# Optimization experiments

Measured on AMD Instinct MI355X. Metric: run time of the kernel, lower is better.

Reference implementation:

```python
import jax, jax.numpy as jnp
import numpy as np

N_NODES = 100000
N_EDGES = 3200000
IN_DIM, HID, OUT = 256, 64, 10


def setup_inputs() -> dict:
    key = jax.random.key(0)
    ks = jax.random.split(key, 6)
    x = jax.random.normal(ks[0], (N_NODES, IN_DIM), jnp.float32)
    edge_index = jax.random.randint(ks[1], (2, N_EDGES), 0, N_NODES, dtype=jnp.int64)
    edge_weight = jnp.ones((N_EDGES,), jnp.float32)
    # Glorot-scaled weights; PyG GCNConv keeps bias separate from lin.
    W1 = jax.random.normal(ks[2], (HID, IN_DIM), jnp.float32) * np.float32(1.0 / np.sqrt(IN_DIM))
    b1 = jnp.zeros((HID,), jnp.float32)
    W2 = jax.random.normal(ks[3], (HID, HID), jnp.float32) * np.float32(1.0 / np.sqrt(HID))
    b2 = jnp.zeros((HID,), jnp.float32)
    W3 = jax.random.normal(ks[4], (OUT, HID), jnp.float32) * np.float32(1.0 / np.sqrt(HID))
    b3 = jnp.zeros((OUT,), jnp.float32)
    return dict(x=x, edge_index=edge_index, edge_weight=edge_weight,
                W1=W1, b1=b1, W2=W2, b2=b2, W3=W3, b3=b3)


def _gcn_conv(x, W, b, row, col, edge_weight, n):
    """PyG GCNConv with add_self_loops=False: out = D^{-1/2} A D^{-1/2} (x W^T) + b."""
    h = x @ W.T  # [N, out_dim]
    deg = jax.ops.segment_sum(edge_weight, col, num_segments=n)  # in-degree by weight
    dinv = jnp.where(deg > 0, jax.lax.rsqrt(jnp.maximum(deg, 1e-12)), 0.0)
    norm = dinv[row] * edge_weight * dinv[col]  # [E]
    msgs = h[row] * norm[:, None]               # gather from source nodes
    out = jax.ops.segment_sum(msgs, col, num_segments=n)  # scatter-add to targets
    return out + b


def reference(x, edge_index, edge_weight, W1, b1, W2, b2, W3, b3):
    row, col = edge_index[0], edge_index[1]
    n = x.shape[0]
    h = jax.nn.relu(_gcn_conv(x, W1, b1, row, col, edge_weight, n))
    h = jax.nn.relu(_gcn_conv(h, W2, b2, row, col, edge_weight, n))
    out = _gcn_conv(h, W3, b3, row, col, edge_weight, n)  # logits, [N, num_classes]
    return out
```

## Files before the change

kernel.cpp:

```cpp
#include <hip/hip_runtime.h>
#include <stddef.h>

typedef __attribute__((ext_vector_type(8))) short bf16x8;
typedef __attribute__((ext_vector_type(4))) float f32x4;

#define NPB 512
#define PB  512

__device__ inline float bf2f(unsigned short u) {
    unsigned int v = ((unsigned int)u) << 16;
    float f;
    __builtin_memcpy(&f, &v, 4);
    return f;
}
__device__ inline unsigned short f2bf(float f) {
    unsigned int v;
    __builtin_memcpy(&v, &f, 4);
    unsigned int r = (v + 0x7FFFu + ((v >> 16) & 1u)) >> 16;
    return (unsigned short)r;
}
__device__ inline float feat(const void* p, long long idx, int isbf) {
    if (isbf) return bf2f(((const unsigned short*)p)[idx]);
    return ((const float*)p)[idx];
}
__device__ inline int clampi(int v, int lo, int hi) {
    return v < lo ? lo : (v > hi ? hi : v);
}

__global__ void detect_kernel(const int* ei, const unsigned short* ew16,
                              const unsigned short* x16, int* flags) {
    __shared__ int s_is64, s_pass;
    if (threadIdx.x == 0) { s_is64 = 1; s_pass = 0; }
    __syncthreads();
    int t = threadIdx.x;
    if (t < 128 && ei[2 * t + 1] != 0) atomicAnd(&s_is64, 0);
    if (t < 64) {
        unsigned short h = x16[t];
        unsigned int expf = (h >> 7) & 0xFF;
        if (h == 0 || (expf >= 112 && expf <= 142)) atomicAdd(&s_pass, 1);
    }
    __syncthreads();
    if (t == 0) {
        flags[0] = s_is64;
        flags[1] = (ew16[0] == 0x3F80) ? 1 : 0;
        flags[2] = (s_pass >= 56) ? 1 : 0;
        flags[3] = 1;
    }
}

__global__ void ones_kernel(const void* ew, int* flags, int E) {
    int i = blockIdx.x * blockDim.x + threadIdx.x;
    int wbf = flags[1];
    int b = i * 4;
    int lim = b + 4 < E ? b + 4 : E;
    bool bad = false;
    for (int k = b; k < lim; k++)
        if (feat(ew, k, wbf) != 1.0f) bad = true;
    if (bad) atomicAnd(&flags[3], 0);
}

__global__ void sentinel_kernel(unsigned short* outp, int n, float val) {
    int i = blockIdx.x * blockDim.x + threadIdx.x;
    if (i < n) outp[i] = f2bf(val);
}

__global__ __launch_bounds__(512) void khist_kernel(const int* ei, const int* flags,
                                                    int* ghist, int E, int n,
                                                    int NB, int chunk) {
    __shared__ int hist[256];
    int blk = blockIdx.x;
    for (int i = threadIdx.x; i < NB; i += blockDim.x) hist[i] = 0;
    __syncthreads();
    int is64 = flags[0];
    int e0 = blk * chunk;
    int e1 = e0 + chunk < E ? e0 + chunk : E;
    for (int e = e0 + (int)threadIdx.x; e < e1; e += blockDim.x) {
        int c = is64 ? ei[2 * (E + e)] : ei[E + e];
        c = clampi(c, 0, n - 1);
        atomicAdd(&hist[c >> 9], 1);
    }
    __syncthreads();
    for (int i = threadIdx.x; i < NB; i += blockDim.x) ghist[blk * NB + i] = hist[i];
}

__global__ __launch_bounds__(512) void koff1_kernel(int* ghist, int* btot, int NB) {
    __shared__ int s[512];
    int b = blockIdx.x;
    int t = threadIdx.x;
    int v = ghist[t * NB + b];
    s[t] = v;
    __syncthreads();
    for (int off = 1; off < 512; off <<= 1) {
        int add = (t >= off) ? s[t - off] : 0;
        __syncthreads();
        s[t] += add;
        __syncthreads();
    }
    ghist[t * NB + b] = s[t] - v;
    if (t == 511) btot[b] = s[511];
}

__global__ __launch_bounds__(256) void koff2_kernel(const int* btot, int* bstart,
                                                    int* row_ptr, int NB, int N, int E) {
    __shared__ int s[256];
    int t = threadIdx.x;
    int v = (t < NB) ? btot[t] : 0;
    s[t] = v;
    __syncthreads();
    for (int off = 1; off < 256; off <<= 1) {
        int add = (t >= off) ? s[t - off] : 0;
        __syncthreads();
        s[t] += add;
        __syncthreads();
    }
    if (t < NB) bstart[t] = s[t] - v;
    if (t == 0) row_ptr[N] = E;
}

__global__ __launch_bounds__(512) void kscatter_kernel(const int* ei, const void* ew,
                                                       const int* flags, const int* ghist,
                                                       const int* bstart,
                                                       unsigned int* ebuf, float* wbuf,
                                                       int E, int n, int NB, int chunk) {
    __shared__ int cur[256];
    int blk = blockIdx.x;
    for (int i = threadIdx.x; i < NB; i += blockDim.x)
        cur[i] = ghist[blk * NB + i] + bstart[i];
    __syncthreads();
    int is64 = flags[0], wbf = flags[1], ones = flags[3];
    int e0 = blk * chunk;
    int e1 = e0 + chunk < E ? e0 + chunk : E;
    for (int e = e0 + (int)threadIdx.x; e < e1; e += blockDim.x) {
        int r = is64 ? ei[2 * e] : ei[e];
        int c = is64 ? ei[2 * (E + e)] : ei[E + e];
        r = clampi(r, 0, n - 1);
        c = clampi(c, 0, n - 1);
        int b = c >> 9;
        int pos = atomicAdd(&cur[b], 1);
        ebuf[pos] = ((unsigned int)(c & 511) << 17) | (unsigned int)r;
        if (!ones) wbuf[pos] = feat(ew, e, wbf);
    }
}

__global__ __launch_bounds__(512) void kcsr_a_kernel(const unsigned int* ebuf,
                                                     const float* wbuf, const int* flags,
                                                     const int* bstart, const int* btot,
                                                     int* row_ptr, float* dinv, int N) {
    __shared__ int cnt[512];
    __shared__ int pre[512];
    __shared__ float wsum[512];
    int b = blockIdx.x;
    int t = threadIdx.x;
    int ones = flags[3];
    cnt[t] = 0;
    wsum[t] = 0.f;
    __syncthreads();
    int bs = bstart[b];
    int be = bs + btot[b];
    for (int i = bs + t; i < be; i += 512) {
        unsigned int p = ebuf[i];
        int cl = (int)(p >> 17);
        atomicAdd(&cnt[cl], 1);
        if (!ones) atomicAdd(&wsum[cl], wbuf[i]);
    }
    __syncthreads();
    int v = cnt[t];
    pre[t] = v;
    __syncthreads();
    for (int off = 1; off < 512; off <<= 1) {
        int add = (t >= off) ? pre[t - off] : 0;
        __syncthreads();
        pre[t] += add;
        __syncthreads();
    }
    int node = b * NPB + t;
    if (node < N) {
        row_ptr[node] = bs + pre[t] - v;
        float d = ones ? (float)v : wsum[t];
        dinv[node] = (d > 0.f) ? rsqrtf(fmaxf(d, 1e-12f)) : 0.f;
    }
}

__global__ __launch_bounds__(512) void kcsr_b_kernel(const unsigned int* ebuf,
                                                     const float* wbuf, const int* flags,
                                                     const int* bstart, const int* btot,
                                                     const int* row_ptr, const float* dinv,
                                                     int2* csr_pack, int N) {
    __shared__ int cur[512];
    __shared__ float dloc[512];
    int b = blockIdx.x;
    int t = threadIdx.x;
    int ones = flags[3];
    int node = b * NPB + t;
    cur[t] = (node < N) ? row_ptr[node] : 0;
    dloc[t] = (node < N) ? dinv[node] : 0.f;
    __syncthreads();
    int bs = bstart[b];
    int be = bs + btot[b];
    for (int i = bs + t; i < be; i += 512) {
        unsigned int p = ebuf[i];
        int cl = (int)(p >> 17);
        int r = (int)(p & 0x1FFFFu);
        float w = ones ? 1.0f : wbuf[i];
        float nv = dinv[r] * w * dloc[cl];
        int pos = atomicAdd(&cur[cl], 1);
        csr_pack[pos] = make_int2(r, __float_as_int(nv));
    }
}

__device__ inline void split8(const float* p, bf16x8& hi, bf16x8& lo) {
    for (int i = 0; i < 8; i++) {
        float v = p[i];
        unsigned short h = f2bf(v);
        hi[i] = (short)h;
        lo[i] = (short)f2bf(v - bf2f(h));
    }
}

__global__ void gemm1_kernel(const void* A, const void* W, const int* flags,
                             unsigned short* C, int M, int K) {
    int wave = threadIdx.x >> 6;
    int l = threadIdx.x & 63;
    int m = l & 15;
    int quad = l >> 4;
    int row0 = blockIdx.x * 16;
    int col0 = wave * 16;
    bool arow_ok = (row0 + m) < M;
    int fb = flags[2];
    f32x4 acc = {0.f, 0.f, 0.f, 0.f};
    bf16x8 zf = {0, 0, 0, 0, 0, 0, 0, 0};
    if (fb) {
        const short* As = (const short*)A;
        const short* Ws = (const short*)W;
        for (int k0 = 0; k0 < K; k0 += 32) {
            bf16x8 a = arow_ok
                ? *(const bf16x8*)(As + (long long)(row0 + m) * K + k0 + quad * 8) : zf;
            bf16x8 b = *(const bf16x8*)(Ws + (long long)(col0 + m) * K + k0 + quad * 8);
            acc = __builtin_amdgcn_mfma_f32_16x16x32_bf16(a, b, acc, 0, 0, 0);
        }
    } else {
        const float* Af = (const float*)A;
        const float* Wf = (const float*)W;
        for (int k0 = 0; k0 < K; k0 += 32) {
            bf16x8 ah = zf, al = zf, wh, wl;
            if (arow_ok)
                split8(Af + (long long)(row0 + m) * K + k0 + quad * 8, ah, al);
            split8(Wf + (long long)(col0 + m) * K + k0 + quad * 8, wh, wl);
            acc = __builtin_amdgcn_mfma_f32_16x16x32_bf16(ah, wh, acc, 0, 0, 0);
            acc = __builtin_amdgcn_mfma_f32_16x16x32_bf16(al, wh, acc, 0, 0, 0);
            acc = __builtin_amdgcn_mfma_f32_16x16x32_bf16(ah, wl, acc, 0, 0, 0);
        }
    }
    for (int r = 0; r < 4; r++) {
        int row = row0 + quad * 4 + r;
        if (row < M) C[(long long)row * 64 + col0 + m] = f2bf(acc[r]);
    }
}

__global__ void gemm2_kernel(const unsigned short* A, const void* W, const int* flags,
                             unsigned short* C, int M) {
    int wave = threadIdx.x >> 6;
    int l = threadIdx.x & 63;
    int m = l & 15;
    int quad = l >> 4;
    int row0 = blockIdx.x * 16;
    int col0 = wave * 16;
    bool arow_ok = (row0 + m) < M;
    int fb = flags[2];
    f32x4 acc = {0.f, 0.f, 0.f, 0.f};
    bf16x8 zf = {0, 0, 0, 0, 0, 0, 0, 0};
    const short* As = (const short*)A;
    for (int k0 = 0; k0 < 64; k0 += 32) {
        bf16x8 a = arow_ok
            ? *(const bf16x8*)(As + (long long)(row0 + m) * 64 + k0 + quad * 8) : zf;
        if (fb) {
            const short* Ws = (const short*)W;
            bf16x8 b = *(const bf16x8*)(Ws + (long long)(col0 + m) * 64 + k0 + quad * 8);
            acc = __builtin_amdgcn_mfma_f32_16x16x32_bf16(a, b, acc, 0, 0, 0);
        } else {
            bf16x8 wh, wl;
            split8((const float*)W + (long long)(col0 + m) * 64 + k0 + quad * 8, wh, wl);
            acc = __builtin_amdgcn_mfma_f32_16x16x32_bf16(a, wh, acc, 0, 0, 0);
            acc = __builtin_amdgcn_mfma_f32_16x16x32_bf16(a, wl, acc, 0, 0, 0);
        }
    }
    for (int r = 0; r < 4; r++) {
        int row = row0 + quad * 4 + r;
        if (row < M) C[(long long)row * 64 + col0 + m] = f2bf(acc[r]);
    }
}

__global__ void gemm3_kernel(const unsigned short* A, const void* W, const int* flags,
                             unsigned short* C, int M) {
    int wv = threadIdx.x >> 6;
    int l = threadIdx.x & 63;
    int m = l & 15;
    int quad = l >> 4;
    int row0 = (blockIdx.x * 4 + wv) * 16;
    bool arow_ok = (row0 + m) < M;
    bool bcol_ok = m < 10;
    int fb = flags[2];
    f32x4 acc = {0.f, 0.f, 0.f, 0.f};
    bf16x8 zf = {0, 0, 0, 0, 0, 0, 0, 0};
    const short* As = (const short*)A;
    for (int k0 = 0; k0 < 64; k0 += 32) {
        bf16x8 a = arow_ok
            ? *(const bf16x8*)(As + (long long)(row0 + m) * 64 + k0 + quad * 8) : zf;
        if (fb) {
            const short* Ws = (const short*)W;
            bf16x8 b = bcol_ok
                ? *(const bf16x8*)(Ws + (long long)m * 64 + k0 + quad * 8) : zf;
            acc = __builtin_amdgcn_mfma_f32_16x16x32_bf16(a, b, acc, 0, 0, 0);
        } else {
            bf16x8 wh = zf, wl = zf;
            if (bcol_ok)
                split8((const float*)W + (long long)m * 64 + k0 + quad * 8, wh, wl);
            acc = __builtin_amdgcn_mfma_f32_16x16x32_bf16(a, wh, acc, 0, 0, 0);
            acc = __builtin_amdgcn_mfma_f32_16x16x32_bf16(a, wl, acc, 0, 0, 0);
        }
    }
    if (bcol_ok) {
        for (int r = 0; r < 4; r++) {
            int row = row0 + quad * 4 + r;
            if (row < M) C[(long long)row * 10 + m] = f2bf(acc[r]);
        }
    }
}

__global__ void agg64_kernel(const unsigned short* h, const void* bias,
                             const int* flags, const int* row_ptr,
                             const int2* cp, unsigned short* outp, int n, int do_relu) {
    int l = threadIdx.x & 63;
    int node = blockIdx.x * 4 + (int)(threadIdx.x >> 6);
    if (node >= n) return;
    int g = l >> 3;
    int j = l & 7;
    int beg = row_ptr[node];
    int end = row_ptr[node + 1];
    float a0 = 0.f, a1 = 0.f, a2 = 0.f, a3 = 0.f;
    float a4 = 0.f, a5 = 0.f, a6 = 0.f, a7 = 0.f;
    for (int e = beg; e < end; e += 8) {
        int ee = e + g;
        if (ee < end) {
            int2 p = cp[ee];
            float nv = __int_as_float(p.y);
            uint4 raw = *(const uint4*)(h + (long long)p.x * 64 + j * 8);
            a0 += nv * __uint_as_float(raw.x << 16);
            a1 += nv * __uint_as_float(raw.x & 0xFFFF0000u);
            a2 += nv * __uint_as_float(raw.y << 16);
            a3 += nv * __uint_as_float(raw.y & 0xFFFF0000u);
            a4 += nv * __uint_as_float(raw.z << 16);
            a5 += nv * __uint_as_float(raw.z & 0xFFFF0000u);
            a6 += nv * __uint_as_float(raw.w << 16);
            a7 += nv * __uint_as_float(raw.w & 0xFFFF0000u);
        }
    }
    for (int mask = 8; mask <= 32; mask <<= 1) {
        a0 += __shfl_xor(a0, mask);
        a1 += __shfl_xor(a1, mask);
        a2 += __shfl_xor(a2, mask);
        a3 += __shfl_xor(a3, mask);
        a4 += __shfl_xor(a4, mask);
        a5 += __shfl_xor(a5, mask);
        a6 += __shfl_xor(a6, mask);
        a7 += __shfl_xor(a7, mask);
    }
    if (g == 0) {
        int fb = flags[2];
        float v0 = a0 + feat(bias, j * 8 + 0, fb);
        float v1 = a1 + feat(bias, j * 8 + 1, fb);
        float v2 = a2 + feat(bias, j * 8 + 2, fb);
        float v3 = a3 + feat(bias, j * 8 + 3, fb);
        float v4 = a4 + feat(bias, j * 8 + 4, fb);
        float v5 = a5 + feat(bias, j * 8 + 5, fb);
        float v6 = a6 + feat(bias, j * 8 + 6, fb);
        float v7 = a7 + feat(bias, j * 8 + 7, fb);
        if (do_relu) {
            v0 = fmaxf(v0, 0.f); v1 = fmaxf(v1, 0.f);
            v2 = fmaxf(v2, 0.f); v3 = fmaxf(v3, 0.f);
            v4 = fmaxf(v4, 0.f); v5 = fmaxf(v5, 0.f);
            v6 = fmaxf(v6, 0.f); v7 = fmaxf(v7, 0.f);
        }
        uint4 pk;
        pk.x = (unsigned int)f2bf(v0) | ((unsigned int)f2bf(v1) << 16);
        pk.y = (unsigned int)f2bf(v2) | ((unsigned int)f2bf(v3) << 16);
        pk.z = (unsigned int)f2bf(v4) | ((unsigned int)f2bf(v5) << 16);
        pk.w = (unsigned int)f2bf(v6) | ((unsigned int)f2bf(v7) << 16);
        *(uint4*)(outp + (long long)node * 64 + j * 8) = pk;
    }
}

__global__ void agg10_kernel(const unsigned short* h, const void* bias,
                             const int* flags, const int* row_ptr,
                             const int2* cp, void* outp, int n) {
    int lane = threadIdx.x & 63;
    int node = blockIdx.x * 4 + (int)(threadIdx.x >> 6);
    if (node >= n) return;
    int beg = row_ptr[node];
    int end = row_ptr[node + 1];
    int active = (lane < 10) ? 1 : 0;
    int li = active ? lane : 0;
    float acc = 0.f;
    int e = beg;
    for (; e + 4 <= end; e += 4) {
        int2 p0 = cp[e + 0], p1 = cp[e + 1], p2 = cp[e + 2], p3 = cp[e + 3];
        float h0 = bf2f(h[(long long)p0.x * 10 + li]);
        float h1 = bf2f(h[(long long)p1.x * 10 + li]);
        float h2 = bf2f(h[(long long)p2.x * 10 + li]);
        float h3 = bf2f(h[(long long)p3.x * 10 + li]);
        acc += __int_as_float(p0.y) * h0 + __int_as_float(p1.y) * h1 +
               __int_as_float(p2.y) * h2 + __int_as_float(p3.y) * h3;
    }
    for (; e < end; e++) {
        int2 p = cp[e];
        acc += __int_as_float(p.y) * bf2f(h[(long long)p.x * 10 + li]);
    }
    if (active) {
        float v = acc + feat(bias, lane, flags[2]);
        if (flags[2]) ((unsigned short*)outp)[(long long)node * 10 + lane] = f2bf(v);
        else          ((float*)outp)[(long long)node * 10 + lane] = v;
    }
}

extern "C" void kernel_launch(void* const* d_in, const int* in_sizes, int n_in,
                              void* d_out, int out_size, void* d_ws, size_t ws_size,
                              hipStream_t stream) {
    const void* x  = d_in[0];
    const int*  ei = (const int*)d_in[1];
    const void* ew = d_in[2];
    const void* W1 = d_in[3];
    const void* b1 = d_in[4];
    const void* W2 = d_in[5];
    const void* b2 = d_in[6];
    const void* W3 = d_in[7];
    const void* b3 = d_in[8];

    const int N = in_sizes[0] / 256;
    const int E = in_sizes[1] / 2;
    const int TB = 256;
    const int NB = (N + NPB - 1) / NPB;
    const int chunk = (E + PB - 1) / PB;

    size_t off = 0;
    size_t o_flags = off; off += 16;
    size_t o_ghist = off; off += (size_t)PB * NB * 4; off = (off + 15) & ~(size_t)15;
    size_t o_btot  = off; off += (size_t)NB * 4;
    size_t o_bst   = off; off += (size_t)NB * 4; off = (off + 15) & ~(size_t)15;
    size_t o_rp    = off; off += (size_t)(N + 1) * 4;
    size_t o_dinv  = off; off += (size_t)N * 4; off = (off + 15) & ~(size_t)15;
    size_t o_pack  = off; off += (size_t)E * 8;
    size_t o_bufA  = off; off += (size_t)N * 64 * 2;
    size_t o_bufB  = off; off += (size_t)N * 64 * 2;
    size_t o_h3    = off; off += (size_t)N * 10 * 2;
    size_t need = off;
    if (ws_size < need || (size_t)E * 4 > (size_t)N * 64 * 2) {
        sentinel_kernel<<<dim3((out_size + TB - 1) / TB), dim3(TB), 0, stream>>>(
            (unsigned short*)d_out, out_size, 250.0f);
        return;
    }
    char* ws = (char*)d_ws;
    int*   flags    = (int*)(ws + o_flags);
    int*   ghist    = (int*)(ws + o_ghist);
    int*   btot     = (int*)(ws + o_btot);
    int*   bstart   = (int*)(ws + o_bst);
    int*   row_ptr  = (int*)(ws + o_rp);
    float* dinv     = (float*)(ws + o_dinv);
    int2*  csr_pack = (int2*)(ws + o_pack);
    unsigned short* bufA  = (unsigned short*)(ws + o_bufA);
    unsigned short* bufB  = (unsigned short*)(ws + o_bufB);
    unsigned short* h3buf = (unsigned short*)(ws + o_h3);
    float*        wbuf = (float*)bufA;
    unsigned int* ebuf = (unsigned int*)bufB;

    dim3 tb(TB);
    dim3 tb512(512);
    dim3 gE4((E / 4 + TB - 1) / TB);
    dim3 g16((N + 15) / 16);
    dim3 g64((N + 63) / 64);
    dim3 gAgg((N + 3) / 4);
    dim3 one(1);

    detect_kernel<<<one, tb, 0, stream>>>(ei, (const unsigned short*)ew,
                                          (const unsigned short*)x, flags);
    ones_kernel<<<gE4, tb, 0, stream>>>(ew, flags, E);
    khist_kernel<<<dim3(PB), tb512, 0, stream>>>(ei, flags, ghist, E, N, NB, chunk);
    koff1_kernel<<<dim3(NB), tb512, 0, stream>>>(ghist, btot, NB);
    koff2_kernel<<<one, tb, 0, stream>>>(btot, bstart, row_ptr, NB, N, E);
    kscatter_kernel<<<dim3(PB), tb512, 0, stream>>>(ei, ew, flags, ghist, bstart,
                                                    ebuf, wbuf, E, N, NB, chunk);
    kcsr_a_kernel<<<dim3(NB), tb512, 0, stream>>>(ebuf, wbuf, flags, bstart, btot,
                                                  row_ptr, dinv, N);
    kcsr_b_kernel<<<dim3(NB), tb512, 0, stream>>>(ebuf, wbuf, flags, bstart, btot,
                                                  row_ptr, dinv, csr_pack, N);

    gemm1_kernel<<<g16, tb, 0, stream>>>(x, W1, flags, bufA, N, 256);
    agg64_kernel<<<gAgg, tb, 0, stream>>>(bufA, b1, flags, row_ptr, csr_pack,
                                          bufB, N, 1);
    gemm2_kernel<<<g16, tb, 0, stream>>>(bufB, W2, flags, bufA, N);
    agg64_kernel<<<gAgg, tb, 0, stream>>>(bufA, b2, flags, row_ptr, csr_pack,
                                          bufB, N, 1);
    gemm3_kernel<<<g64, tb, 0, stream>>>(bufB, W3, flags, h3buf, N);
    agg10_kernel<<<gAgg, tb, 0, stream>>>(h3buf, b3, flags, row_ptr, csr_pack,
                                          d_out, N);
}
```

Measured before the change: 660.0 us.

## Pre-split weights to bf16 hi/lo and compute all output columns per wave

Adds a small kernel that splits each weight matrix into bf16 hi/lo halves once per call, instead of re-splitting fp32 weights inside every GEMM wave. The three GEMMs are reorganized so each wave owns 16 rows and computes all 64 output columns with four accumulators. As a result, the fp32 input row (256 wide in layer 1) is loaded and split once rather than once per column-wave. The cost is three extra small launches, extra workspace, and more accumulator registers per thread.

```diff
diff --git a/kernel.cpp b/kernel.cpp
--- a/kernel.cpp
+++ b/kernel.cpp
@@ -3,6 +3,7 @@
 
 typedef __attribute__((ext_vector_type(8))) short bf16x8;
 typedef __attribute__((ext_vector_type(4))) float f32x4;
+typedef __attribute__((ext_vector_type(8))) float f32x8;
 
 #define NPB 512
 #define PB  512
@@ -62,6 +63,22 @@
 __global__ void sentinel_kernel(unsigned short* outp, int n, float val) {
     int i = blockIdx.x * blockDim.x + threadIdx.x;
     if (i < n) outp[i] = f2bf(val);
+}
+
+__global__ void wsplit_kernel(const void* W, const int* flags, unsigned short* hi,
+                              unsigned short* lo, int n_in, int n_out) {
+    int i = blockIdx.x * blockDim.x + threadIdx.x;
+    if (i >= n_out) return;
+    if (i >= n_in) { hi[i] = 0; lo[i] = 0; return; }
+    if (flags[2]) {
+        hi[i] = ((const unsigned short*)W)[i];
+        lo[i] = 0;
+    } else {
+        float v = ((const float*)W)[i];
+        unsigned short h = f2bf(v);
+        hi[i] = h;
+        lo[i] = f2bf(v - bf2f(h));
+    }
 }
 
 __global__ __launch_bounds__(512) void khist_kernel(const int* ei, const int* flags,
@@ -208,118 +225,139 @@
     }
 }
 
-__device__ inline void split8(const float* p, bf16x8& hi, bf16x8& lo) {
+__device__ inline void split8v(f32x8 v, bf16x8& hi, bf16x8& lo) {
     for (int i = 0; i < 8; i++) {
-        float v = p[i];
-        unsigned short h = f2bf(v);
+        float f = v[i];
+        unsigned short h = f2bf(f);
         hi[i] = (short)h;
-        lo[i] = (short)f2bf(v - bf2f(h));
-    }
-}
-
-__global__ void gemm1_kernel(const void* A, const void* W, const int* flags,
-                             unsigned short* C, int M, int K) {
+        lo[i] = (short)f2bf(f - bf2f(h));
+    }
+}
+
+__global__ __launch_bounds__(256) void gemm1_kernel(const void* A,
+                             const unsigned short* Whi, const unsigned short* Wlo,
+                             const int* flags, unsigned short* C, int M, int K) {
     int wave = threadIdx.x >> 6;
     int l = threadIdx.x & 63;
     int m = l & 15;
     int quad = l >> 4;
-    int row0 = blockIdx.x * 16;
-    int col0 = wave * 16;
+    int row0 = blockIdx.x * 64 + wave * 16;
     bool arow_ok = (row0 + m) < M;
     int fb = flags[2];
-    f32x4 acc = {0.f, 0.f, 0.f, 0.f};
+    f32x4 acc[4];
+    #pragma unroll
+    for (int n = 0; n < 4; n++) acc[n] = (f32x4){0.f, 0.f, 0.f, 0.f};
     bf16x8 zf = {0, 0, 0, 0, 0, 0, 0, 0};
+    long long abase = (long long)(row0 + m) * K + quad * 8;
     if (fb) {
         const short* As = (const short*)A;
-        const short* Ws = (const short*)W;
+        #pragma unroll 4
         for (int k0 = 0; k0 < K; k0 += 32) {
-            bf16x8 a = arow_ok
-                ? *(const bf16x8*)(As + (long long)(row0 + m) * K + k0 + quad * 8) : zf;
-            bf16x8 b = *(const bf16x8*)(Ws + (long long)(col0 + m) * K + k0 + quad * 8);
-            acc = __builtin_amdgcn_mfma_f32_16x16x32_bf16(a, b, acc, 0, 0, 0);
+            bf16x8 a = arow_ok ? *(const bf16x8*)(As + abase + k0) : zf;
+            #pragma unroll
+            for (int n = 0; n < 4; n++) {
+                const unsigned short* wp = Whi + (long long)(n * 16 + m) * K + k0 + quad * 8;
+                bf16x8 b = *(const bf16x8*)wp;
+                acc[n] = __builtin_amdgcn_mfma_f32_16x16x32_bf16(a, b, acc[n], 0, 0, 0);
+            }
         }
     } else {
         const float* Af = (const float*)A;
-        const float* Wf = (const float*)W;
+        #pragma unroll 2
         for (int k0 = 0; k0 < K; k0 += 32) {
-            bf16x8 ah = zf, al = zf, wh, wl;
-            if (arow_ok)
-                split8(Af + (long long)(row0 + m) * K + k0 + quad * 8, ah, al);
-            split8(Wf + (long long)(col0 + m) * K + k0 + quad * 8, wh, wl);
-            acc = __builtin_amdgcn_mfma_f32_16x16x32_bf16(ah, wh, acc, 0, 0, 0);
-            acc = __builtin_amdgcn_mfma_f32_16x16x32_bf16(al, wh, acc, 0, 0, 0);
-            acc = __builtin_amdgcn_mfma_f32_16x16x32_bf16(ah, wl, acc, 0, 0, 0);
-        }
-    }
-    for (int r = 0; r < 4; r++) {
-        int row = row0 + quad * 4 + r;
-        if (row < M) C[(long long)row * 64 + col0 + m] = f2bf(acc[r]);
-    }
-}
-
-__global__ void gemm2_kernel(const unsigned short* A, const void* W, const int* flags,
-                             unsigned short* C, int M) {
+            bf16x8 ah = zf, al = zf;
+            if (arow_ok) {
+                f32x8 av = *(const f32x8*)(Af + abase + k0);
+                split8v(av, ah, al);
+            }
+            #pragma unroll
+            for (int n = 0; n < 4; n++) {
+                long long widx = (long long)(n * 16 + m) * K + k0 + quad * 8;
+                bf16x8 wh = *(const bf16x8*)(Whi + widx);
+                bf16x8 wl = *(const bf16x8*)(Wlo + widx);
+                acc[n] = __builtin_amdgcn_mfma_f32_16x16x32_bf16(ah, wh, acc[n], 0, 0, 0);
+                acc[n] = __builtin_amdgcn_mfma_f32_16x16x32_bf16(al, wh, acc[n], 0, 0, 0);
+                acc[n] = __builtin_amdgcn_mfma_f32_16x16x32_bf16(ah, wl, acc[n], 0, 0, 0);
+            }
+        }
+    }
+    #pragma unroll
+    for (int n = 0; n < 4; n++) {
+        #pragma unroll
+        for (int r = 0; r < 4; r++) {
+            int row = row0 + quad * 4 + r;
+            if (row < M) C[(long long)row * 64 + n * 16 + m] = f2bf(acc[n][r]);
+        }
+    }
+}
+
+__global__ __launch_bounds__(256) void gemm2_kernel(const unsigned short* A,
+                             const unsigned short* Whi, const unsigned short* Wlo,
+                             const int* flags, unsigned short* C, int M) {
     int wave = threadIdx.x >> 6;
     int l = threadIdx.x & 63;
     int m = l & 15;
     int quad = l >> 4;
-    int row0 = blockIdx.x * 16;
-    int col0 = wave * 16;
+    int row0 = blockIdx.x * 64 + wave * 16;
+    bool arow_ok = (row0 + m) < M;
+    int fb = flags[2];
+    f32x4 acc[4];
+    #pragma unroll
+    for (int n = 0; n < 4; n++) acc[n] = (f32x4){0.f, 0.f, 0.f, 0.f};
+    bf16x8 zf = {0, 0, 0, 0, 0, 0, 0, 0};
+    const short* As = (const short*)A;
+    long long abase = (long long)(row0 + m) * 64 + quad * 8;
+    #pragma unroll
+    for (int k0 = 0; k0 < 64; k0 += 32) {
+        bf16x8 a = arow_ok ? *(const bf16x8*)(As + abase + k0) : zf;
+        #pragma unroll
+        for (int n = 0; n < 4; n++) {
+            long long widx = (long long)(n * 16 + m) * 64 + k0 + quad * 8;
+            bf16x8 wh = *(const bf16x8*)(Whi + widx);
+            acc[n] = __builtin_amdgcn_mfma_f32_16x16x32_bf16(a, wh, acc[n], 0, 0, 0);
+            if (!fb) {
+                bf16x8 wl = *(const bf16x8*)(Wlo + widx);
+                acc[n] = __builtin_amdgcn_mfma_f32_16x16x32_bf16(a, wl, acc[n], 0, 0, 0);
+            }
+        }
+    }
+    #pragma unroll
+    for (int n = 0; n < 4; n++) {
+        #pragma unroll
+        for (int r = 0; r < 4; r++) {
+            int row = row0 + quad * 4 + r;
+            if (row < M) C[(long long)row * 64 + n * 16 + m] = f2bf(acc[n][r]);
+        }
+    }
+}
+
+__global__ __launch_bounds__(256) void gemm3_kernel(const unsigned short* A,
+                             const unsigned short* Whi, const unsigned short* Wlo,
+                             const int* flags, unsigned short* C, int M) {
+    int wave = threadIdx.x >> 6;
+    int l = threadIdx.x & 63;
+    int m = l & 15;
+    int quad = l >> 4;
+    int row0 = blockIdx.x * 64 + wave * 16;
     bool arow_ok = (row0 + m) < M;
     int fb = flags[2];
     f32x4 acc = {0.f, 0.f, 0.f, 0.f};
     bf16x8 zf = {0, 0, 0, 0, 0, 0, 0, 0};
     const short* As = (const short*)A;
+    long long abase = (long long)(row0 + m) * 64 + quad * 8;
+    #pragma unroll
     for (int k0 = 0; k0 < 64; k0 += 32) {
-        bf16x8 a = arow_ok
-            ? *(const bf16x8*)(As + (long long)(row0 + m) * 64 + k0 + quad * 8) : zf;
-        if (fb) {
-            const short* Ws = (const short*)W;
-            bf16x8 b = *(const bf16x8*)(Ws + (long long)(col0 + m) * 64 + k0 + quad * 8);
-            acc = __builtin_amdgcn_mfma_f32_16x16x32_bf16(a, b, acc, 0, 0, 0);
-        } else {
-            bf16x8 wh, wl;
-            split8((const float*)W + (long long)(col0 + m) * 64 + k0 + quad * 8, wh, wl);
-            acc = __builtin_amdgcn_mfma_f32_16x16x32_bf16(a, wh, acc, 0, 0, 0);
+        bf16x8 a = arow_ok ? *(const bf16x8*)(As + abase + k0) : zf;
+        long long widx = (long long)m * 64 + k0 + quad * 8;
+        bf16x8 wh = *(const bf16x8*)(Whi + widx);
+        acc = __builtin_amdgcn_mfma_f32_16x16x32_bf16(a, wh, acc, 0, 0, 0);
+        if (!fb) {
+            bf16x8 wl = *(const bf16x8*)(Wlo + widx);
             acc = __builtin_amdgcn_mfma_f32_16x16x32_bf16(a, wl, acc, 0, 0, 0);
         }
     }
-    for (int r = 0; r < 4; r++) {
-        int row = row0 + quad * 4 + r;
-        if (row < M) C[(long long)row * 64 + col0 + m] = f2bf(acc[r]);
-    }
-}
-
-__global__ void gemm3_kernel(const unsigned short* A, const void* W, const int* flags,
-                             unsigned short* C, int M) {
-    int wv = threadIdx.x >> 6;
-    int l = threadIdx.x & 63;
-    int m = l & 15;
-    int quad = l >> 4;
-    int row0 = (blockIdx.x * 4 + wv) * 16;
-    bool arow_ok = (row0 + m) < M;
-    bool bcol_ok = m < 10;
-    int fb = flags[2];
-    f32x4 acc = {0.f, 0.f, 0.f, 0.f};
-    bf16x8 zf = {0, 0, 0, 0, 0, 0, 0, 0};
-    const short* As = (const short*)A;
-    for (int k0 = 0; k0 < 64; k0 += 32) {
-        bf16x8 a = arow_ok
-            ? *(const bf16x8*)(As + (long long)(row0 + m) * 64 + k0 + quad * 8) : zf;
-        if (fb) {
-            const short* Ws = (const short*)W;
-            bf16x8 b = bcol_ok
-                ? *(const bf16x8*)(Ws + (long long)m * 64 + k0 + quad * 8) : zf;
-            acc = __builtin_amdgcn_mfma_f32_16x16x32_bf16(a, b, acc, 0, 0, 0);
-        } else {
-            bf16x8 wh = zf, wl = zf;
-            if (bcol_ok)
-                split8((const float*)W + (long long)m * 64 + k0 + quad * 8, wh, wl);
-            acc = __builtin_amdgcn_mfma_f32_16x16x32_bf16(a, wh, acc, 0, 0, 0);
-            acc = __builtin_amdgcn_mfma_f32_16x16x32_bf16(a, wl, acc, 0, 0, 0);
-        }
-    }
-    if (bcol_ok) {
+    if (m < 10) {
+        #pragma unroll
         for (int r = 0; r < 4; r++) {
             int row = row0 + quad * 4 + r;
             if (row < M) C[(long long)row * 10 + m] = f2bf(acc[r]);
@@ -451,7 +489,13 @@
     size_t o_pack  = off; off += (size_t)E * 8;
     size_t o_bufA  = off; off += (size_t)N * 64 * 2;
     size_t o_bufB  = off; off += (size_t)N * 64 * 2;
-    size_t o_h3    = off; off += (size_t)N * 10 * 2;
+    size_t o_h3    = off; off += (size_t)N * 10 * 2; off = (off + 15) & ~(size_t)15;
+    size_t o_w1hi  = off; off += (size_t)64 * 256 * 2;
+    size_t o_w1lo  = off; off += (size_t)64 * 256 * 2;
+    size_t o_w2hi  = off; off += (size_t)64 * 64 * 2;
+    size_t o_w2lo  = off; off += (size_t)64 * 64 * 2;
+    size_t o_w3hi  = off; off += (size_t)16 * 64 * 2;
+    size_t o_w3lo  = off; off += (size_t)16 * 64 * 2;
     size_t need = off;
     if (ws_size < need || (size_t)E * 4 > (size_t)N * 64 * 2) {
         sentinel_kernel<<<dim3((out_size + TB - 1) / TB), dim3(TB), 0, stream>>>(
@@ -469,19 +513,30 @@
     unsigned short* bufA  = (unsigned short*)(ws + o_bufA);
     unsigned short* bufB  = (unsigned short*)(ws + o_bufB);
     unsigned short* h3buf = (unsigned short*)(ws + o_h3);
+    unsigned short* w1hi  = (unsigned short*)(ws + o_w1hi);
+    unsigned short* w1lo  = (unsigned short*)(ws + o_w1lo);
+    unsigned short* w2hi  = (unsigned short*)(ws + o_w2hi);
+    unsigned short* w2lo  = (unsigned short*)(ws + o_w2lo);
+    unsigned short* w3hi  = (unsigned short*)(ws + o_w3hi);
+    unsigned short* w3lo  = (unsigned short*)(ws + o_w3lo);
     float*        wbuf = (float*)bufA;
     unsigned int* ebuf = (unsigned int*)bufB;
 
     dim3 tb(TB);
     dim3 tb512(512);
     dim3 gE4((E / 4 + TB - 1) / TB);
-    dim3 g16((N + 15) / 16);
-    dim3 g64((N + 63) / 64);
+    dim3 gG((N + 63) / 64);
     dim3 gAgg((N + 3) / 4);
     dim3 one(1);
 
     detect_kernel<<<one, tb, 0, stream>>>(ei, (const unsigned short*)ew,
                                           (const unsigned short*)x, flags);
+    wsplit_kernel<<<dim3(64), tb, 0, stream>>>(W1, flags, w1hi, w1lo,
+                                               64 * 256, 64 * 256);
+    wsplit_kernel<<<dim3(16), tb, 0, stream>>>(W2, flags, w2hi, w2lo,
+                                               64 * 64, 64 * 64);
+    wsplit_kernel<<<dim3(4), tb, 0, stream>>>(W3, flags, w3hi, w3lo,
+                                              10 * 64, 16 * 64);
     ones_kernel<<<gE4, tb, 0, stream>>>(ew, flags, E);
     khist_kernel<<<dim3(PB), tb512, 0, stream>>>(ei, flags, ghist, E, N, NB, chunk);
     koff1_kernel<<<dim3(NB), tb512, 0, stream>>>(ghist, btot, NB);
@@ -493,13 +548,13 @@
     kcsr_b_kernel<<<dim3(NB), tb512, 0, stream>>>(ebuf, wbuf, flags, bstart, btot,
                                                   row_ptr, dinv, csr_pack, N);
 
-    gemm1_kernel<<<g16, tb, 0, stream>>>(x, W1, flags, bufA, N, 256);
+    gemm1_kernel<<<gG, tb, 0, stream>>>(x, w1hi, w1lo, flags, bufA, N, 256);
     agg64_kernel<<<gAgg, tb, 0, stream>>>(bufA, b1, flags, row_ptr, csr_pack,
                                           bufB, N, 1);
-    gemm2_kernel<<<g16, tb, 0, stream>>>(bufB, W2, flags, bufA, N);
+    gemm2_kernel<<<gG, tb, 0, stream>>>(bufB, w2hi, w2lo, flags, bufA, N);
     agg64_kernel<<<gAgg, tb, 0, stream>>>(bufA, b2, flags, row_ptr, csr_pack,
                                           bufB, N, 1);
-    gemm3_kernel<<<g64, tb, 0, stream>>>(bufB, W3, flags, h3buf, N);
+    gemm3_kernel<<<gG, tb, 0, stream>>>(bufB, w3hi, w3lo, flags, h3buf, N);
     agg10_kernel<<<gAgg, tb, 0, stream>>>(h3buf, b3, flags, row_ptr, csr_pack,
                                           d_out, N);
 }
```

New measurement: 641.9 us. 2.7% less time.
